# Kernel optimization log

Hardware: AMD Instinct MI355X
Metric: run time of the kernel (lower is better)

The kernel has to match this reference:

```python
import jax, jax.numpy as jnp
import numpy as np

WIN = 7
N = WIN * WIN  # 49 tokens per window
C = 384
H = 12
HD = C // H
B_ = 4096
NW = 64  # number of distinct window masks; must divide B_


def _relative_position_index(wh=WIN, ww=WIN):
    coords = np.stack(np.meshgrid(np.arange(wh), np.arange(ww), indexing='ij'))  # [2,wh,ww]
    cf = coords.reshape(2, -1)
    rel = cf[:, :, None] - cf[:, None, :]               # [2,N,N]
    rel = rel.transpose(1, 2, 0).astype(np.int32)       # [N,N,2]
    rel[:, :, 0] += wh - 1
    rel[:, :, 1] += ww - 1
    rel[:, :, 0] *= 2 * ww - 1
    return jnp.asarray(rel.sum(-1))                     # [N,N] int32


def setup_inputs() -> dict:
    key = jax.random.key(0)
    ks = jax.random.split(key, 8)
    std = 0.02
    return {
        'x': jax.random.normal(ks[0], (B_, N, C), jnp.float32),
        'mask': jnp.zeros((NW, N, N), jnp.float32),  # 0/-inf mask; zeros here
        'qkv_w': jax.random.normal(ks[1], (3 * C, C), jnp.float32) * std,
        'qkv_b': jnp.zeros((3 * C,), jnp.float32),
        'rpb_table': jax.random.normal(ks[2], ((2 * WIN - 1) ** 2, H), jnp.float32) * std,
        'proj_l_w': jax.random.normal(ks[3], (H, H), jnp.float32) * std,
        'proj_l_b': jnp.zeros((H,), jnp.float32),
        'proj_w_w': jax.random.normal(ks[4], (H, H), jnp.float32) * std,
        'proj_w_b': jnp.zeros((H,), jnp.float32),
        'proj_weight': jax.random.normal(ks[5], (C, C), jnp.float32) * std,
        'proj_bias': jnp.zeros((C,), jnp.float32),
        'rel_index': _relative_position_index(),
    }


def reference(x, mask, qkv_w, qkv_b, rpb_table, proj_l_w, proj_l_b,
              proj_w_w, proj_w_b, proj_weight, proj_bias, rel_index):
    B, n, c = x.shape
    scale = HD ** (-0.5)
    qkv = x @ qkv_w.T + qkv_b                     # [B,N,3C]
    q_out, k_out, v_out = jnp.split(qkv, 3, axis=-1)  # each [B,N,C]
    qkv5 = qkv.reshape(B, n, 3, H, HD)
    q = qkv5[:, :, 0].transpose(0, 2, 1, 3)       # [B,H,N,hd]
    k = qkv5[:, :, 1].transpose(0, 2, 1, 3)
    v = qkv5[:, :, 2].transpose(0, 2, 1, 3)
    attn = jnp.einsum('bhnd,bhmd->bhnm', q * scale, k)   # [B,H,N,N]
    bias = rpb_table[rel_index]                   # [N,N,H]
    attn = attn + bias.transpose(2, 0, 1)[None]
    # proj_l: linear mixing across heads (Linear acts on last dim after permute)
    attn = jnp.einsum('bhnm,gh->bgnm', attn, proj_l_w) + proj_l_b[None, :, None, None]
    nW = mask.shape[0]
    attn = attn.reshape(B // nW, nW, H, n, n) + mask[None, :, None]
    attn = attn.reshape(B, H, n, n)
    attn = jax.nn.softmax(attn, axis=-1)
    # proj_w: head mixing after softmax
    attn = jnp.einsum('bhnm,gh->bgnm', attn, proj_w_w) + proj_w_b[None, :, None, None]
    out = jnp.einsum('bhnm,bhmd->bnhd', attn, v).reshape(B, n, c)
    out = out @ proj_weight.T + proj_bias
    return (out, (q_out, k_out, v_out))
```

## Files before the change

kernel.cpp:

```cpp
#include <hip/hip_runtime.h>
#include <hip/hip_bf16.h>

#define TOK 49
#define NPT 2401
#define CDIM 384
#define NH 12
#define HDIM 32
#define NWIN 64
#define BTOT 4096
#define OUTSZ (BTOT * TOK * CDIM)
#define L2E 1.4426950408889634f

typedef __attribute__((ext_vector_type(8))) short bf16x8;
typedef __attribute__((ext_vector_type(4))) float f32x4;
typedef unsigned int uint32;
typedef unsigned short ushort_t;

__device__ inline ushort_t f2bf(float f) {
  uint32 u = __float_as_uint(f);
  u += 0x7FFF + ((u >> 16) & 1);
  return (ushort_t)(u >> 16);
}
__device__ inline uint32 pk2(float a, float b) {
  union { __hip_bfloat162 h; uint32 u; } x;
  x.h = __float22bfloat162_rn(float2{a, b});
  return x.u;
}
__device__ inline float bf2f(uint32 u) { return __uint_as_float((u & 0xffffu) << 16); }
__device__ inline bf16x8 pack8(float4 a, float4 b) {
  union { __hip_bfloat162 h[4]; bf16x8 v; } u;
  u.h[0] = __float22bfloat162_rn(float2{a.x, a.y});
  u.h[1] = __float22bfloat162_rn(float2{a.z, a.w});
  u.h[2] = __float22bfloat162_rn(float2{b.x, b.y});
  u.h[3] = __float22bfloat162_rn(float2{b.z, b.w});
  return u.v;
}
__device__ inline bf16x8 pack8f(const float* f) {
  union { __hip_bfloat162 h[4]; bf16x8 v; } u;
#pragma unroll
  for (int i = 0; i < 4; ++i) u.h[i] = __float22bfloat162_rn(float2{f[2*i], f[2*i+1]});
  return u.v;
}

__global__ void k_cvt(const float* __restrict__ src, ushort_t* __restrict__ dst, int n8) {
  int i = blockIdx.x * 256 + threadIdx.x;
  if (i >= n8) return;
  const float4* s = (const float4*)(src + (size_t)i * 8);
  float4 a = s[0], b = s[1];
  uint4 o;
  o.x = (uint32)f2bf(a.x) | ((uint32)f2bf(a.y) << 16);
  o.y = (uint32)f2bf(a.z) | ((uint32)f2bf(a.w) << 16);
  o.z = (uint32)f2bf(b.x) | ((uint32)f2bf(b.y) << 16);
  o.w = (uint32)f2bf(b.z) | ((uint32)f2bf(b.w) << 16);
  *(uint4*)(dst + (size_t)i * 8) = o;
}

__global__ void k_bias(const float* __restrict__ rpb, const float* __restrict__ plw,
                       const float* __restrict__ plb, float* __restrict__ bm) {
  int i = blockIdx.x * 256 + threadIdx.x;
  if (i >= 169 * 16) return;
  int rid = i >> 4, g = i & 15;
  float s = 0.f;
  if (g < NH) {
    s = plb[g];
#pragma unroll
    for (int h = 0; h < NH; ++h) s = fmaf(plw[g * NH + h], rpb[rid * NH + h], s);
    s *= L2E;
  }
  bm[i] = s;
}

__launch_bounds__(256)
__global__ void k_qkv_mfma(const ushort_t* __restrict__ Xb, const ushort_t* __restrict__ Wb,
                           const float* __restrict__ Bq, float* __restrict__ qslab) {
  __shared__ ushort_t As[128 * 32];
  __shared__ ushort_t Bs[128 * 32];
  const int tid = threadIdx.x;
  const int l = tid & 63;
  const int wv = tid >> 6;
  const int wr = wv >> 1, wc = wv & 1;
  const int row0 = blockIdx.x * 128;
  const int col0 = blockIdx.y * 128;

  f32x4 acc[4][4];
#pragma unroll
  for (int i = 0; i < 4; ++i)
#pragma unroll
    for (int j = 0; j < 4; ++j)
#pragma unroll
      for (int e = 0; e < 4; ++e) acc[i][j][e] = 0.f;

  for (int kb = 0; kb < CDIM; kb += 32) {
#pragma unroll
    for (int i = 0; i < 2; ++i) {
      int cid = tid + i * 256;
      int r = cid >> 2, c = cid & 3;
      uint4 v = *(const uint4*)&Xb[(size_t)(row0 + r) * CDIM + kb + c * 8];
      *(uint4*)&As[r * 32 + c * 8] = v;
      uint4 w = *(const uint4*)&Wb[(size_t)(col0 + r) * CDIM + kb + c * 8];
      *(uint4*)&Bs[r * 32 + c * 8] = w;
    }
    __syncthreads();
    bf16x8 af[4], bfr[4];
#pragma unroll
    for (int mt = 0; mt < 4; ++mt)
      af[mt] = *(const bf16x8*)&As[(wr * 64 + mt * 16 + (l & 15)) * 32 + (l >> 4) * 8];
#pragma unroll
    for (int nt = 0; nt < 4; ++nt)
      bfr[nt] = *(const bf16x8*)&Bs[(wc * 64 + nt * 16 + (l & 15)) * 32 + (l >> 4) * 8];
#pragma unroll
    for (int mt = 0; mt < 4; ++mt)
#pragma unroll
      for (int nt = 0; nt < 4; ++nt)
        acc[mt][nt] = __builtin_amdgcn_mfma_f32_16x16x32_bf16(af[mt], bfr[nt], acc[mt][nt], 0, 0, 0);
    __syncthreads();
  }

  const int slab = blockIdx.y / 3;
  const int cslab0 = col0 - slab * CDIM;
  float* dst = qslab + (size_t)slab * OUTSZ;
#pragma unroll
  for (int nt = 0; nt < 4; ++nt) {
    int colg = col0 + wc * 64 + nt * 16 + (l & 15);
    int colo = cslab0 + wc * 64 + nt * 16 + (l & 15);
    float bv = Bq[colg];
#pragma unroll
    for (int mt = 0; mt < 4; ++mt) {
      int rbase = row0 + wr * 64 + mt * 16 + (l >> 4) * 4;
#pragma unroll
      for (int j = 0; j < 4; ++j)
        dst[(size_t)(rbase + j) * CDIM + colo] = acc[mt][nt][j] + bv;
    }
  }
}

__launch_bounds__(1024, 8)
__global__ void k_attn8(const float* __restrict__ qslab, const float* __restrict__ kslab,
                        const float* __restrict__ vslab, const float* __restrict__ mask,
                        const float* __restrict__ bmg, const int* __restrict__ relidx,
                        const float* __restrict__ plw, const float* __restrict__ pww,
                        const float* __restrict__ pwb, float* __restrict__ xout) {
  __shared__ __align__(16) ushort_t SA[1240 * 16];
  __shared__ __align__(16) ushort_t PP[12 * 1400 + 416];
  __shared__ __align__(16) ushort_t bm16[169 * 12 + 4];
  __shared__ ushort_t ridx_s[1240];

  const int tid = threadIdx.x;
  const int b  = blockIdx.x >> 1;
  const int bh = blockIdx.x & 1;
  const int n0 = bh * 25;
  const int NR = bh ? 24 : 25;
  const size_t base = (size_t)b * TOK * CDIM;
  const int l = tid & 63, l15 = l & 15, l16 = l >> 4;
  const int wv = tid >> 6;
  const float SCL = 0.17677669529663687f * L2E;

  for (int i = tid; i < 169 * 12; i += 1024) {
    int rid = i / 12, g = i - rid * 12;
    bm16[i] = f2bf(bmg[rid * 16 + g]);
  }
  for (int i = tid; i < 1240; i += 1024) {
    int pg = i + n0 * 49; if (pg > 2400) pg = 2400;
    ridx_s[i] = (ushort_t)relidx[pg];
  }
  for (int p = tid; p < 1240; p += 1024) *(uint2*)&SA[p * 16 + 12] = uint2{0u, 0u};
  if (tid < 512) *(uint32*)&SA[1176 * 16 + tid * 2] = 0u;
  if (tid < 208) *(uint32*)&PP[12 * 1400 + tid * 2] = 0u;

  {
    const int art = wv >> 3;
    const int act = (wv >> 1) & 3;
    const int ah0 = (wv & 1) * 6;
    const int nrow = art * 16 + l15;
    const int mrow = act * 16 + l15;
    const bool qv = nrow < NR;
    const bool kv = mrow < TOK;
#pragma unroll
    for (int hp = 0; hp < 3; ++hp) {
      f32x4 s2[2];
#pragma unroll
      for (int hh = 0; hh < 2; ++hh) {
        int h = ah0 + hp * 2 + hh;
        bf16x8 af = {0,0,0,0,0,0,0,0}, bf = {0,0,0,0,0,0,0,0};
        if (qv) {
          const float4* qp = (const float4*)(qslab + base + (size_t)(n0 + nrow) * CDIM + h * HDIM + l16 * 8);
          af = pack8(qp[0], qp[1]);
        }
        if (kv) {
          const float4* kp = (const float4*)(kslab + base + (size_t)mrow * CDIM + h * HDIM + l16 * 8);
          bf = pack8(kp[0], kp[1]);
        }
        f32x4 z = {0.f, 0.f, 0.f, 0.f};
        s2[hh] = __builtin_amdgcn_mfma_f32_16x16x32_bf16(af, bf, z, 0, 0, 0);
      }
#pragma unroll
      for (int j = 0; j < 4; ++j) {
        int nj = art * 16 + l16 * 4 + j;
        if (nj < NR && kv)
          *(uint32*)&SA[(nj * 49 + mrow) * 16 + ah0 + hp * 2] = pk2(s2[0][j], s2[1][j]);
      }
    }
  }
  __syncthreads();

  {
    const float* maskw = mask + (size_t)(b & (NWIN - 1)) * NPT;
    float apf[8], bpf[8];
#pragma unroll
    for (int j = 0; j < 8; ++j) {
      int kj = l16 * 8 + j;
      apf[j] = (l15 < NH && kj < NH) ? plw[l15 * NH + kj] * SCL : 0.f;
      bpf[j] = (l15 < NH && kj < NH) ? pww[l15 * NH + kj] : 0.f;
    }
    const bf16x8 aplw = pack8f(apf);
    const bf16x8 bpww = pack8f(bpf);
    const float pwbv = (l15 < NH) ? pwb[l15] : 0.f;

    for (int nl = wv; nl < NR; nl += 16) {
      const int pb0 = nl * 49;
      float ev[4][4];
      float rs[4] = {0.f, 0.f, 0.f, 0.f};
#pragma unroll
      for (int mc = 0; mc < 4; ++mc) {
        int m = mc * 16 + l15;
        int pl = pb0 + m;
        bf16x8 sf = {0,0,0,0,0,0,0,0};
        if (l16 < 2) sf = *(const bf16x8*)&SA[pl * 16 + l16 * 8];
        int rid = (int)ridx_s[pl];
        uint2 bmu = *(const uint2*)&bm16[rid * 12 + l16 * 4];
        int pg = pl + n0 * 49; if (pg > 2400) pg = 2400;
        float mk = maskw[pg] * L2E;
        f32x4 cini = {bf2f(bmu.x) + mk, bf2f(bmu.x >> 16) + mk,
                      bf2f(bmu.y) + mk, bf2f(bmu.y >> 16) + mk};
        f32x4 o = __builtin_amdgcn_mfma_f32_16x16x32_bf16(aplw, sf, cini, 0, 0, 0);
        bool okm = (m < TOK);
#pragma unroll
        for (int j = 0; j < 4; ++j) {
          int g = l16 * 4 + j;
          float e = (okm && g < NH) ? exp2f(o[j]) : 0.f;
          ev[mc][j] = e;
          rs[j] += e;
        }
      }
#pragma unroll
      for (int d = 1; d < 16; d <<= 1)
#pragma unroll
        for (int j = 0; j < 4; ++j) rs[j] += __shfl_xor(rs[j], d, 64);
      float inv[4];
#pragma unroll
      for (int j = 0; j < 4; ++j) inv[j] = (rs[j] > 0.f) ? 1.f / rs[j] : 0.f;

#pragma unroll
      for (int mc = 0; mc < 4; ++mc) {
        int m = mc * 16 + l15;
        if (m < TOK) {
          uint2 w;
          w.x = pk2(ev[mc][0] * inv[0], ev[mc][1] * inv[1]);
          w.y = pk2(ev[mc][2] * inv[2], ev[mc][3] * inv[3]);
          *(uint2*)&SA[(pb0 + m) * 16 + l16 * 4] = w;
        }
      }
#pragma unroll
      for (int mc = 0; mc < 4; ++mc) {
        bf16x8 pf8 = {0,0,0,0,0,0,0,0};
        if (l16 < 2) pf8 = *(const bf16x8*)&SA[(pb0 + mc * 16 + l15) * 16 + l16 * 8];
        f32x4 cd = {pwbv, pwbv, pwbv, pwbv};
        f32x4 o = __builtin_amdgcn_mfma_f32_16x16x32_bf16(pf8, bpww, cd, 0, 0, 0);
        int m0 = mc * 16 + l16 * 4;
        if (l15 < NH && m0 < 56) {
          float z0 = (m0     < TOK) ? o[0] : 0.f;
          float z1 = (m0 + 1 < TOK) ? o[1] : 0.f;
          float z2 = (m0 + 2 < TOK) ? o[2] : 0.f;
          float z3 = (m0 + 3 < TOK) ? o[3] : 0.f;
          uint2 w;
          w.x = pk2(z0, z1);
          w.y = pk2(z2, z3);
          *(uint2*)&PP[l15 * 1400 + nl * 56 + m0] = w;
        }
      }
    }
  }
  __syncthreads();

  {
    const int ert = wv >> 3;
    const int edt = (wv >> 2) & 1;
    const int egq = wv & 3;
#pragma unroll
    for (int gi = 0; gi < 3; ++gi) {
      int g = egq * 3 + gi;
      int col = g * HDIM + edt * 16 + l15;
      f32x4 acc = {0.f, 0.f, 0.f, 0.f};
#pragma unroll
      for (int ks = 0; ks < 2; ++ks) {
        bf16x8 pa8 = {0,0,0,0,0,0,0,0};
        if (!(ks == 1 && l16 == 3))
          pa8 = *(const bf16x8*)&PP[g * 1400 + (ert * 16 + l15) * 56 + ks * 32 + l16 * 8];
        float vf[8];
#pragma unroll
        for (int e = 0; e < 8; ++e) {
          int m = ks * 32 + l16 * 8 + e;
          vf[e] = (m < TOK) ? vslab[base + (size_t)m * CDIM + col] : 0.f;
        }
        bf16x8 vb8 = pack8f(vf);
        acc = __builtin_amdgcn_mfma_f32_16x16x32_bf16(pa8, vb8, acc, 0, 0, 0);
      }
#pragma unroll
      for (int j = 0; j < 4; ++j) {
        int nlo = ert * 16 + l16 * 4 + j;
        if (nlo < NR)
          xout[base + (size_t)(n0 + nlo) * CDIM + col] = acc[j];
      }
    }
  }
}

__launch_bounds__(512, 4)
__global__ void k_proj3(float* __restrict__ Y, const float* __restrict__ W,
                        const float* __restrict__ Bv) {
  __shared__ __align__(16) ushort_t Asb[64 * 392];
  __shared__ __align__(16) ushort_t Bsb[384 * 40];
  const int tid = threadIdx.x;
  const int l = tid & 63, l15 = l & 15, l16 = l >> 4;
  const int wv = tid >> 6;
  const int wr = wv >> 2;
  const int wc = wv & 3;
  const int row0 = blockIdx.x * 64;

#pragma unroll
  for (int i = 0; i < 6; ++i) {
    int cid = tid + i * 512;
    int r = cid / 48, c8 = cid - (cid / 48) * 48;
    const float4* s = (const float4*)&Y[(size_t)(row0 + r) * CDIM + c8 * 8];
    float4 a = s[0], b = s[1];
    uint4 o;
    o.x = pk2(a.x, a.y); o.y = pk2(a.z, a.w);
    o.z = pk2(b.x, b.y); o.w = pk2(b.z, b.w);
    *(uint4*)&Asb[r * 392 + c8 * 8] = o;
  }

  f32x4 acc[2][6];
#pragma unroll
  for (int i = 0; i < 2; ++i)
#pragma unroll
    for (int j = 0; j < 6; ++j)
#pragma unroll
      for (int e = 0; e < 4; ++e) acc[i][j][e] = 0.f;

  for (int kb = 0; kb < 12; ++kb) {
    __syncthreads();
#pragma unroll
    for (int i = 0; i < 3; ++i) {
      int cid = tid + i * 512;
      int col = cid >> 2, k8 = cid & 3;
      const float4* s = (const float4*)&W[(size_t)col * CDIM + kb * 32 + k8 * 8];
      float4 a = s[0], b = s[1];
      uint4 o;
      o.x = pk2(a.x, a.y); o.y = pk2(a.z, a.w);
      o.z = pk2(b.x, b.y); o.w = pk2(b.z, b.w);
      *(uint4*)&Bsb[col * 40 + k8 * 8] = o;
    }
    __syncthreads();
    bf16x8 af[2], bfr[6];
#pragma unroll
    for (int mt = 0; mt < 2; ++mt)
      af[mt] = *(const bf16x8*)&Asb[(wr * 32 + mt * 16 + l15) * 392 + kb * 32 + l16 * 8];
#pragma unroll
    for (int nt = 0; nt < 6; ++nt)
      bfr[nt] = *(const bf16x8*)&Bsb[(wc * 96 + nt * 16 + l15) * 40 + l16 * 8];
#pragma unroll
    for (int mt = 0; mt < 2; ++mt)
#pragma unroll
      for (int nt = 0; nt < 6; ++nt)
        acc[mt][nt] = __builtin_amdgcn_mfma_f32_16x16x32_bf16(af[mt], bfr[nt], acc[mt][nt], 0, 0, 0);
  }

#pragma unroll
  for (int nt = 0; nt < 6; ++nt) {
    int col = wc * 96 + nt * 16 + l15;
    float bv = Bv[col];
#pragma unroll
    for (int mt = 0; mt < 2; ++mt) {
      int rbase = row0 + wr * 32 + mt * 16 + l16 * 4;
#pragma unroll
      for (int j = 0; j < 4; ++j)
        Y[(size_t)(rbase + j) * CDIM + col] = acc[mt][nt][j] + bv;
    }
  }
}

extern "C" void kernel_launch(void* const* d_in, const int* in_sizes, int n_in,
                              void* d_out, int out_size, void* d_ws, size_t ws_size,
                              hipStream_t stream) {
  const float* x      = (const float*)d_in[0];
  const float* mask   = (const float*)d_in[1];
  const float* qkv_w  = (const float*)d_in[2];
  const float* qkv_b  = (const float*)d_in[3];
  const float* rpb    = (const float*)d_in[4];
  const float* plw    = (const float*)d_in[5];
  const float* plb    = (const float*)d_in[6];
  const float* pww    = (const float*)d_in[7];
  const float* pwb    = (const float*)d_in[8];
  const float* projw  = (const float*)d_in[9];
  const float* projb  = (const float*)d_in[10];
  const int*   relidx = (const int*)d_in[11];

  float* out   = (float*)d_out;
  float* qslab = out + (size_t)OUTSZ;
  float* kslab = out + 2 * (size_t)OUTSZ;
  float* vslab = out + 3 * (size_t)OUTSZ;

  ushort_t* Xb = (ushort_t*)out;
  ushort_t* Wb = (ushort_t*)(out + 70000000);
  float*    bm = (float*)d_ws;

  k_cvt<<<(OUTSZ / 8 + 255) / 256, 256, 0, stream>>>(x, Xb, OUTSZ / 8);
  k_cvt<<<(3 * CDIM * CDIM / 8 + 255) / 256, 256, 0, stream>>>(qkv_w, Wb, 3 * CDIM * CDIM / 8);
  k_bias<<<(169 * 16 + 255) / 256, 256, 0, stream>>>(rpb, plw, plb, bm);

  dim3 g1(BTOT * TOK / 128, (3 * CDIM) / 128);
  k_qkv_mfma<<<g1, 256, 0, stream>>>(Xb, Wb, qkv_b, qslab);

  k_attn8<<<BTOT * 2, 1024, 0, stream>>>(qslab, kslab, vslab, mask, bm, relidx,
                                         plw, pww, pwb, out);

  k_proj3<<<BTOT * TOK / 64, 512, 0, stream>>>(out, projw, projb);
}
```

Baseline: 1.507 ms.

## Stage V transposed in LDS for PV MFMA and swizzle QKV GEMM block order

The attention kernel now loads the window's V rows once with coalesced reads, converts them to bf16 and stores them transposed in shared memory (reusing the SA buffer, enlarged). The PV MFMA then reads its operands from LDS instead of issuing strided per-element global loads. The QKV GEMM switches to a 1D grid with an XCD-aware swizzle so that consecutive blocks land on the same die and share L2. The cost is an extra barrier and an LDS staging pass per block, with some risk of bank conflicts on the 52-element stride.

After: 1.350 ms. -10.4%, faster.

```diff
diff --git a/kernel.cpp b/kernel.cpp
--- a/kernel.cpp
+++ b/kernel.cpp
@@ -75,12 +75,16 @@
                            const float* __restrict__ Bq, float* __restrict__ qslab) {
   __shared__ ushort_t As[128 * 32];
   __shared__ ushort_t Bs[128 * 32];
+  const int bid = blockIdx.x;
+  const int sw = (bid & 7) * 1764 + (bid >> 3);
+  const int bx = sw / 9;
+  const int by = sw - bx * 9;
   const int tid = threadIdx.x;
   const int l = tid & 63;
   const int wv = tid >> 6;
   const int wr = wv >> 1, wc = wv & 1;
-  const int row0 = blockIdx.x * 128;
-  const int col0 = blockIdx.y * 128;
+  const int row0 = bx * 128;
+  const int col0 = by * 128;
 
   f32x4 acc[4][4];
 #pragma unroll
@@ -116,7 +120,7 @@
     __syncthreads();
   }
 
-  const int slab = blockIdx.y / 3;
+  const int slab = by / 3;
   const int cslab0 = col0 - slab * CDIM;
   float* dst = qslab + (size_t)slab * OUTSZ;
 #pragma unroll
@@ -135,12 +139,12 @@
 }
 
 __launch_bounds__(1024, 8)
-__global__ void k_attn8(const float* __restrict__ qslab, const float* __restrict__ kslab,
+__global__ void k_attn9(const float* __restrict__ qslab, const float* __restrict__ kslab,
                         const float* __restrict__ vslab, const float* __restrict__ mask,
                         const float* __restrict__ bmg, const int* __restrict__ relidx,
                         const float* __restrict__ plw, const float* __restrict__ pww,
                         const float* __restrict__ pwb, float* __restrict__ xout) {
-  __shared__ __align__(16) ushort_t SA[1240 * 16];
+  __shared__ __align__(16) ushort_t SA[19976];
   __shared__ __align__(16) ushort_t PP[12 * 1400 + 416];
   __shared__ __align__(16) ushort_t bm16[169 * 12 + 4];
   __shared__ ushort_t ridx_s[1240];
@@ -164,7 +168,7 @@
     ridx_s[i] = (ushort_t)relidx[pg];
   }
   for (int p = tid; p < 1240; p += 1024) *(uint2*)&SA[p * 16 + 12] = uint2{0u, 0u};
-  if (tid < 512) *(uint32*)&SA[1176 * 16 + tid * 2] = 0u;
+  if (tid < 580) *(uint32*)&SA[18816 + tid * 2] = 0u;
   if (tid < 208) *(uint32*)&PP[12 * 1400 + tid * 2] = 0u;
 
   {
@@ -283,6 +287,24 @@
   __syncthreads();
 
   {
+    ushort_t* Vt = SA;
+    for (int i = tid; i < CDIM * 13; i += 1024) {
+      int mq = i / CDIM, c = i - mq * CDIM;
+      int m = mq * 4;
+      float f0 = (m     < TOK) ? vslab[base + (size_t)(m    ) * CDIM + c] : 0.f;
+      float f1 = (m + 1 < TOK) ? vslab[base + (size_t)(m + 1) * CDIM + c] : 0.f;
+      float f2 = (m + 2 < TOK) ? vslab[base + (size_t)(m + 2) * CDIM + c] : 0.f;
+      float f3 = (m + 3 < TOK) ? vslab[base + (size_t)(m + 3) * CDIM + c] : 0.f;
+      uint2 u;
+      u.x = pk2(f0, f1);
+      u.y = pk2(f2, f3);
+      *(uint2*)&Vt[c * 52 + mq * 4] = u;
+    }
+  }
+  __syncthreads();
+
+  {
+    const ushort_t* Vt = SA;
     const int ert = wv >> 3;
     const int edt = (wv >> 2) & 1;
     const int egq = wv & 3;
@@ -294,15 +316,15 @@
 #pragma unroll
       for (int ks = 0; ks < 2; ++ks) {
         bf16x8 pa8 = {0,0,0,0,0,0,0,0};
-        if (!(ks == 1 && l16 == 3))
+        bf16x8 vb8 = {0,0,0,0,0,0,0,0};
+        if (!(ks == 1 && l16 == 3)) {
           pa8 = *(const bf16x8*)&PP[g * 1400 + (ert * 16 + l15) * 56 + ks * 32 + l16 * 8];
-        float vf[8];
-#pragma unroll
-        for (int e = 0; e < 8; ++e) {
-          int m = ks * 32 + l16 * 8 + e;
-          vf[e] = (m < TOK) ? vslab[base + (size_t)m * CDIM + col] : 0.f;
-        }
-        bf16x8 vb8 = pack8f(vf);
+          uint2 lo = *(const uint2*)&Vt[col * 52 + ks * 32 + l16 * 8];
+          uint2 hi = *(const uint2*)&Vt[col * 52 + ks * 32 + l16 * 8 + 4];
+          union { uint32 u[4]; bf16x8 v; } uv;
+          uv.u[0] = lo.x; uv.u[1] = lo.y; uv.u[2] = hi.x; uv.u[3] = hi.y;
+          vb8 = uv.v;
+        }
         acc = __builtin_amdgcn_mfma_f32_16x16x32_bf16(pa8, vb8, acc, 0, 0, 0);
       }
 #pragma unroll
@@ -418,10 +440,9 @@
   k_cvt<<<(3 * CDIM * CDIM / 8 + 255) / 256, 256, 0, stream>>>(qkv_w, Wb, 3 * CDIM * CDIM / 8);
   k_bias<<<(169 * 16 + 255) / 256, 256, 0, stream>>>(rpb, plw, plb, bm);
 
-  dim3 g1(BTOT * TOK / 128, (3 * CDIM) / 128);
-  k_qkv_mfma<<<g1, 256, 0, stream>>>(Xb, Wb, qkv_b, qslab);
-
-  k_attn8<<<BTOT * 2, 1024, 0, stream>>>(qslab, kslab, vslab, mask, bm, relidx,
+  k_qkv_mfma<<<(BTOT * TOK / 128) * 9, 256, 0, stream>>>(Xb, Wb, qkv_b, qslab);
+
+  k_attn9<<<BTOT * 2, 1024, 0, stream>>>(qslab, kslab, vslab, mask, bm, relidx,
                                          plw, pww, pwb, out);
 
   k_proj3<<<BTOT * TOK / 64, 512, 0, stream>>>(out, projw, projb);
```
